# Kernel optimization log

Hardware: AMD Instinct MI355X
Metric: run time of the kernel (lower is better)

Reference implementation:

```python
import jax, jax.numpy as jnp
import numpy as np

B, S, D = 64, 1452, 1024
G, K, R = 288, 4, 32
VIS = 1152  # number of vision patch tokens; tail is S - VIS = 300 text tokens
MAX_TOKENS = 300


def setup_inputs() -> dict:
    key = jax.random.key(0)
    k1, k2, k3, k4 = jax.random.split(key, 4)
    hidden_states = jax.random.normal(k1, (B, S, D), dtype=jnp.float32)
    attention_mask = jnp.ones((B, S), dtype=jnp.int32)
    # all batches share the same vision patch range [0, VIS-1]
    patch_range_list = jnp.tile(jnp.array([[0, VIS - 1]], dtype=jnp.int32), (B, 1))
    base = jnp.broadcast_to(jnp.arange(VIS, dtype=jnp.int32).reshape(1, G, K), (B, G, K))
    drop = jax.random.uniform(k2, (B, G, K)) < 0.1
    patch_indices_list_list = jnp.where(drop, jnp.int32(-1), base)
    rem = jax.random.randint(k3, (B, R), 0, VIS, dtype=jnp.int32)
    rem = jnp.where(jax.random.uniform(k4, (B, R)) < 0.25, jnp.int32(-1), rem)
    return {
        "hidden_states": hidden_states,
        "attention_mask": attention_mask,
        "patch_range_list": patch_range_list,
        "patch_indices_list_list": patch_indices_list_list,
        "remove_index_list_list": rem,
    }


def reference(hidden_states, attention_mask, patch_range_list, patch_indices_list_list, remove_index_list_list):
    Bn, Sn, Dn = hidden_states.shape
    _, Gn, Kn = patch_indices_list_list.shape
    # vision_end_token_index is taken from batch 0 in the original and used for a
    # shape-defining slice; treat as static (identical across batches here).
    vis_end = int(patch_range_list[0, 1]) + 1

    start = patch_range_list[:, 0]            # [B]
    end = patch_range_list[:, 1]              # [B]
    L = end - start + 1                       # [B] length of sliced hidden_state

    idx = patch_indices_list_list             # [B,G,K]
    mask = idx != -1                          # [B,G,K]
    # remove_index_list: drop -1 padding (map to -2 sentinel so it never matches)
    rem = jnp.where(remove_index_list_list == -1, jnp.int32(-2), remove_index_list_list)  # [B,R]
    in_rem = (idx[..., None] == rem[:, None, None, :]).any(-1)  # torch.isin, [B,G,K]
    mask = mask & ~in_rem

    # torch gather with -1 wraps to the last element of the SLICED hidden_state;
    # replicate exactly (note: the original sums wrapped/removed entries too).
    idx_w = jnp.where(idx >= 0, idx, idx + L[:, None, None])
    gidx = start[:, None, None] + idx_w       # absolute indices into hidden_states
    gathered = jnp.take_along_axis(
        hidden_states, gidx.reshape(Bn, Gn * Kn, 1), axis=1
    ).reshape(Bn, Gn, Kn, Dn)

    cnt = mask.sum(-1)                        # [B,G] divisor = count of kept entries
    pooled = gathered.sum(2) / jnp.maximum(cnt, 1)[..., None].astype(hidden_states.dtype)

    # rows with no valid entries are dropped; survivors are written right-aligned
    valid = mask.any(-1)                      # [B,G]
    n_valid = valid.sum(1)                    # [B]
    rank = jnp.cumsum(valid, axis=1) - 1      # 0-based rank among valid rows
    pos = jnp.where(valid, MAX_TOKENS - n_valid[:, None] + rank, MAX_TOKENS)  # OOB -> drop
    bidx = jnp.arange(Bn)[:, None]

    out_head = jnp.zeros((Bn, MAX_TOKENS, Dn), hidden_states.dtype).at[bidx, pos].set(pooled, mode="drop")
    att_head = jnp.zeros((Bn, MAX_TOKENS), attention_mask.dtype).at[bidx, pos].set(1, mode="drop")

    outputs = jnp.concatenate([out_head, hidden_states[:, vis_end:]], axis=1)
    outputs_attention = jnp.concatenate([att_head, attention_mask[:, vis_end:]], axis=1)
    return outputs, outputs_attention
```

## Files before the change

kernel.cpp:

```cpp
#include <hip/hip_runtime.h>
#include <hip/hip_bf16.h>

#define Bn 64
#define Sn 1452
#define Dn 1024
#define Gn 288
#define Kn 4
#define Rn 32
#define MAXT 300

typedef float f32x4 __attribute__((ext_vector_type(4)));

__global__ void __launch_bounds__(512)
phaseA_kernel(const int* __restrict__ idx,
              const int* __restrict__ rem,
              const int* __restrict__ attn,
              int* __restrict__ cnt_ws,
              int* __restrict__ gor_ws,
              int* __restrict__ nv_ws,
              float* __restrict__ att_out,
              int vis_end, int T) {
    const int b = blockIdx.x;
    const int tid = threadIdx.x;

    __shared__ int s_rem[Rn];
    __shared__ int s_wsum[8];

    if (tid < Rn) {
        int r = rem[b * Rn + tid];
        s_rem[tid] = (r == -1) ? -2 : r;
    }
    __syncthreads();

    int cnt = 0;
    if (tid < Gn) {
#pragma unroll
        for (int k = 0; k < Kn; ++k) {
            int v = idx[(b * Gn + tid) * Kn + k];
            bool m = (v != -1);
            if (m) {
#pragma unroll
                for (int r = 0; r < Rn; ++r) {
                    if (v == s_rem[r]) { m = false; }
                }
            }
            cnt += m ? 1 : 0;
        }
        cnt_ws[b * Gn + tid] = cnt;
    }

    const int valid = (tid < Gn && cnt > 0) ? 1 : 0;
    const unsigned long long m = __ballot(valid);
    const int lane = tid & 63;
    const int w = tid >> 6;
    if (lane == 0) s_wsum[w] = __popcll(m);
    __syncthreads();

    int off = 0, tot = 0;
#pragma unroll
    for (int i = 0; i < 8; ++i) {
        int v = s_wsum[i];
        tot += v;
        if (i < w) off += v;
    }
    if (valid) {
        int rank = off + __popcll(m & ((1ull << lane) - 1ull));
        gor_ws[b * Gn + rank] = tid;
    }
    if (tid == 0) nv_ws[b] = tot;

    const int nvalid = tot;
    for (int t = tid; t < T; t += 512) {
        float v;
        if (t < MAXT) {
            v = (t >= MAXT - nvalid) ? 1.0f : 0.0f;
        } else {
            v = (float)attn[b * Sn + vis_end + (t - MAXT)];
        }
        att_out[(size_t)b * T + t] = v;
    }
}

__global__ void __launch_bounds__(256)
rows_kernel(const float* __restrict__ hs,
            const int* __restrict__ idx,
            const int* __restrict__ pr,
            const int* __restrict__ cnt_ws,
            const int* __restrict__ gor_ws,
            const int* __restrict__ nv_ws,
            float* __restrict__ out,
            int vis_end, int T, int nheadblk, int tail4) {
    const int x = blockIdx.x;
    const int b = blockIdx.y;
    const int tid = threadIdx.x;

    if (x >= nheadblk) {
        const int c = x - nheadblk;
        const f32x4* src = (const f32x4*)(hs + ((size_t)b * Sn + vis_end) * Dn);
        f32x4* dst = (f32x4*)(out + ((size_t)b * T + MAXT) * Dn);

        const int base = c * 1024;
        f32x4 v0, v1, v2, v3;
        int e0 = base + 0 * 256 + tid;
        int e1 = base + 1 * 256 + tid;
        int e2 = base + 2 * 256 + tid;
        int e3 = base + 3 * 256 + tid;
        bool p0 = e0 < tail4, p1 = e1 < tail4, p2 = e2 < tail4, p3 = e3 < tail4;
        if (p0) v0 = __builtin_nontemporal_load(&src[e0]);
        if (p1) v1 = __builtin_nontemporal_load(&src[e1]);
        if (p2) v2 = __builtin_nontemporal_load(&src[e2]);
        if (p3) v3 = __builtin_nontemporal_load(&src[e3]);
        if (p0) __builtin_nontemporal_store(v0, &dst[e0]);
        if (p1) __builtin_nontemporal_store(v1, &dst[e1]);
        if (p2) __builtin_nontemporal_store(v2, &dst[e2]);
        if (p3) __builtin_nontemporal_store(v3, &dst[e3]);
        return;
    }

    const int nvalid = nv_ws[b];
    const int zcut = MAXT - nvalid;
    const int start = pr[b * 2];
    const int L = pr[b * 2 + 1] - start + 1;

#pragma unroll
    for (int i = 0; i < 2; ++i) {
        const int t = 2 * x + i;
        if (t >= MAXT) break;
        f32x4* outp = (f32x4*)(out + ((size_t)b * T + t) * Dn);
        if (t < zcut) {
            f32x4 z = {0.f, 0.f, 0.f, 0.f};
            __builtin_nontemporal_store(z, &outp[tid]);
            continue;
        }
        const int g = gor_ws[b * Gn + (t - zcut)];
        f32x4 acc = {0.f, 0.f, 0.f, 0.f};
#pragma unroll
        for (int k = 0; k < Kn; ++k) {
            int v = idx[(b * Gn + g) * Kn + k];
            int w = (v >= 0) ? v : v + L;
            const f32x4* row = (const f32x4*)(hs + ((size_t)b * Sn + start + w) * Dn);
            acc += row[tid];
        }
        const int c = cnt_ws[b * Gn + g];
        const float scale = 1.0f / (float)((c > 1) ? c : 1);
        acc *= scale;
        __builtin_nontemporal_store(acc, &outp[tid]);
    }
}

extern "C" void kernel_launch(void* const* d_in, const int* in_sizes, int n_in,
                              void* d_out, int out_size, void* d_ws, size_t ws_size,
                              hipStream_t stream) {
    const float* hs  = (const float*)d_in[0];
    const int* attn  = (const int*)d_in[1];
    const int* pr    = (const int*)d_in[2];
    const int* idx   = (const int*)d_in[3];
    const int* rem   = (const int*)d_in[4];

    float* out = (float*)d_out;

    const int T = out_size / (Bn * (Dn + 1));
    const int vis_end = Sn - (T - MAXT);

    float* att_out = out + (size_t)Bn * T * Dn;

    int* cnt_ws = (int*)d_ws;
    int* gor_ws = cnt_ws + Bn * Gn;
    int* nv_ws  = gor_ws + Bn * Gn;

    const int tail_rows = T - MAXT;
    const int tail4 = tail_rows * (Dn / 4);
    const int ntail = (tail_rows + 3) / 4;
    const int nheadblk = (MAXT + 1) / 2;

    phaseA_kernel<<<Bn, 512, 0, stream>>>(idx, rem, attn, cnt_ws, gor_ws, nv_ws,
                                          att_out, vis_end, T);
    rows_kernel<<<dim3(nheadblk + ntail, Bn), 256, 0, stream>>>(
        hs, idx, pr, cnt_ws, gor_ws, nv_ws, out, vis_end, T, nheadblk, tail4);
}
```

Baseline: 83.05 us.

## Fuse mask/rank computation into row kernel, recomputing per block in shared memory

Removes the separate phase-A kernel and its global workspace by having every head block recompute the per-batch keep counts, validity ballots and compacted group order in shared memory, then gather and pool its two rows. Tail-copy blocks now also write the attention-mask tail. This eliminates one launch and the inter-kernel dependency, but each of the 150 head blocks per batch redundantly runs the 288x4x32 remove-index comparison and adds two barriers before its memory work.

```diff
diff --git a/kernel.cpp b/kernel.cpp
--- a/kernel.cpp
+++ b/kernel.cpp
@@ -11,94 +11,28 @@
 
 typedef float f32x4 __attribute__((ext_vector_type(4)));
 
-__global__ void __launch_bounds__(512)
-phaseA_kernel(const int* __restrict__ idx,
+__global__ void __launch_bounds__(256)
+fused2_kernel(const float* __restrict__ hs,
+              const int* __restrict__ idx,
+              const int* __restrict__ pr,
               const int* __restrict__ rem,
               const int* __restrict__ attn,
-              int* __restrict__ cnt_ws,
-              int* __restrict__ gor_ws,
-              int* __restrict__ nv_ws,
+              float* __restrict__ out,
               float* __restrict__ att_out,
-              int vis_end, int T) {
-    const int b = blockIdx.x;
-    const int tid = threadIdx.x;
-
-    __shared__ int s_rem[Rn];
-    __shared__ int s_wsum[8];
-
-    if (tid < Rn) {
-        int r = rem[b * Rn + tid];
-        s_rem[tid] = (r == -1) ? -2 : r;
-    }
-    __syncthreads();
-
-    int cnt = 0;
-    if (tid < Gn) {
-#pragma unroll
-        for (int k = 0; k < Kn; ++k) {
-            int v = idx[(b * Gn + tid) * Kn + k];
-            bool m = (v != -1);
-            if (m) {
-#pragma unroll
-                for (int r = 0; r < Rn; ++r) {
-                    if (v == s_rem[r]) { m = false; }
-                }
-            }
-            cnt += m ? 1 : 0;
-        }
-        cnt_ws[b * Gn + tid] = cnt;
-    }
-
-    const int valid = (tid < Gn && cnt > 0) ? 1 : 0;
-    const unsigned long long m = __ballot(valid);
-    const int lane = tid & 63;
-    const int w = tid >> 6;
-    if (lane == 0) s_wsum[w] = __popcll(m);
-    __syncthreads();
-
-    int off = 0, tot = 0;
-#pragma unroll
-    for (int i = 0; i < 8; ++i) {
-        int v = s_wsum[i];
-        tot += v;
-        if (i < w) off += v;
-    }
-    if (valid) {
-        int rank = off + __popcll(m & ((1ull << lane) - 1ull));
-        gor_ws[b * Gn + rank] = tid;
-    }
-    if (tid == 0) nv_ws[b] = tot;
-
-    const int nvalid = tot;
-    for (int t = tid; t < T; t += 512) {
-        float v;
-        if (t < MAXT) {
-            v = (t >= MAXT - nvalid) ? 1.0f : 0.0f;
-        } else {
-            v = (float)attn[b * Sn + vis_end + (t - MAXT)];
-        }
-        att_out[(size_t)b * T + t] = v;
-    }
-}
-
-__global__ void __launch_bounds__(256)
-rows_kernel(const float* __restrict__ hs,
-            const int* __restrict__ idx,
-            const int* __restrict__ pr,
-            const int* __restrict__ cnt_ws,
-            const int* __restrict__ gor_ws,
-            const int* __restrict__ nv_ws,
-            float* __restrict__ out,
-            int vis_end, int T, int nheadblk, int tail4) {
+              int vis_end, int T, int nheadblk, int tail4, int tailrows) {
     const int x = blockIdx.x;
     const int b = blockIdx.y;
     const int tid = threadIdx.x;
 
     if (x >= nheadblk) {
         const int c = x - nheadblk;
+        if (tid < 4) {
+            int tr = c * 4 + tid;
+            if (tr < tailrows)
+                att_out[(size_t)b * T + MAXT + tr] = (float)attn[b * Sn + vis_end + tr];
+        }
         const f32x4* src = (const f32x4*)(hs + ((size_t)b * Sn + vis_end) * Dn);
         f32x4* dst = (f32x4*)(out + ((size_t)b * T + MAXT) * Dn);
-
         const int base = c * 1024;
         f32x4 v0, v1, v2, v3;
         int e0 = base + 0 * 256 + tid;
@@ -117,34 +51,102 @@
         return;
     }
 
-    const int nvalid = nv_ws[b];
+    __shared__ int s_rem[Rn];
+    __shared__ unsigned long long s_mask[5];
+    __shared__ int s_wsum[5];
+    __shared__ short s_gor[Gn];
+    __shared__ char s_cnt[Gn];
+
+    const int lane = tid & 63;
+    const int w = tid >> 6;
+
+    if (tid < Rn) {
+        int r = rem[b * Rn + tid];
+        s_rem[tid] = (r == -1) ? -2 : r;
+    }
+    __syncthreads();
+
+    int cnt1 = 0;
+    {
+        const int g = tid;
+#pragma unroll
+        for (int k = 0; k < Kn; ++k) {
+            int v = idx[(b * Gn + g) * Kn + k];
+            bool m = (v != -1);
+#pragma unroll
+            for (int r = 0; r < Rn; ++r) m = m && (v != s_rem[r]);
+            cnt1 += m ? 1 : 0;
+        }
+        s_cnt[g] = (char)cnt1;
+    }
+    int cnt2 = 0;
+    if (tid < Gn - 256) {
+        const int g = 256 + tid;
+#pragma unroll
+        for (int k = 0; k < Kn; ++k) {
+            int v = idx[(b * Gn + g) * Kn + k];
+            bool m = (v != -1);
+#pragma unroll
+            for (int r = 0; r < Rn; ++r) m = m && (v != s_rem[r]);
+            cnt2 += m ? 1 : 0;
+        }
+        s_cnt[g] = (char)cnt2;
+    }
+
+    unsigned long long m1 = __ballot(cnt1 > 0);
+    if (lane == 0) { s_mask[w] = m1; s_wsum[w] = __popcll(m1); }
+    if (w == 0) {
+        unsigned long long m2 = __ballot(tid < Gn - 256 && cnt2 > 0);
+        if (lane == 0) { s_mask[4] = m2; s_wsum[4] = __popcll(m2); }
+    }
+    __syncthreads();
+
+    int pre[5], acc = 0;
+#pragma unroll
+    for (int i = 0; i < 5; ++i) { pre[i] = acc; acc += s_wsum[i]; }
+    const int nvalid = acc;
     const int zcut = MAXT - nvalid;
+
+    if (cnt1 > 0) {
+        int rank = pre[w] + __popcll(s_mask[w] & ((1ull << lane) - 1ull));
+        s_gor[rank] = (short)tid;
+    }
+    if (tid < Gn - 256 && cnt2 > 0) {
+        int rank = pre[4] + __popcll(s_mask[4] & ((1ull << lane) - 1ull));
+        s_gor[rank] = (short)(256 + tid);
+    }
+    __syncthreads();
+
+    if (tid < 2) {
+        int t = 2 * x + tid;
+        att_out[(size_t)b * T + t] = (t >= zcut) ? 1.0f : 0.0f;
+    }
+
     const int start = pr[b * 2];
     const int L = pr[b * 2 + 1] - start + 1;
 
 #pragma unroll
     for (int i = 0; i < 2; ++i) {
         const int t = 2 * x + i;
-        if (t >= MAXT) break;
         f32x4* outp = (f32x4*)(out + ((size_t)b * T + t) * Dn);
         if (t < zcut) {
             f32x4 z = {0.f, 0.f, 0.f, 0.f};
             __builtin_nontemporal_store(z, &outp[tid]);
             continue;
         }
-        const int g = gor_ws[b * Gn + (t - zcut)];
-        f32x4 acc = {0.f, 0.f, 0.f, 0.f};
+        const int g = s_gor[t - zcut];
+        f32x4 a = {0.f, 0.f, 0.f, 0.f};
 #pragma unroll
         for (int k = 0; k < Kn; ++k) {
             int v = idx[(b * Gn + g) * Kn + k];
-            int w = (v >= 0) ? v : v + L;
-            const f32x4* row = (const f32x4*)(hs + ((size_t)b * Sn + start + w) * Dn);
-            acc += row[tid];
+            int wi = (v >= 0) ? v : v + L;
+            const f32x4* row = (const f32x4*)(hs + ((size_t)b * Sn + start + wi) * Dn);
+            a += row[tid];
         }
-        const int c = cnt_ws[b * Gn + g];
+        const int c = (int)s_cnt[g];
         const float scale = 1.0f / (float)((c > 1) ? c : 1);
-        acc *= scale;
-        __builtin_nontemporal_store(acc, &outp[tid]);
+        a *= scale;
+        __builtin_nontemporal_store(a, &outp[tid]);
     }
 }
 
@@ -164,17 +166,11 @@
 
     float* att_out = out + (size_t)Bn * T * Dn;
 
-    int* cnt_ws = (int*)d_ws;
-    int* gor_ws = cnt_ws + Bn * Gn;
-    int* nv_ws  = gor_ws + Bn * Gn;
-
-    const int tail_rows = T - MAXT;
-    const int tail4 = tail_rows * (Dn / 4);
-    const int ntail = (tail_rows + 3) / 4;
+    const int tailrows = T - MAXT;
+    const int tail4 = tailrows * (Dn / 4);
+    const int ntail = (tailrows + 3) / 4;
     const int nheadblk = (MAXT + 1) / 2;
 
-    phaseA_kernel<<<Bn, 512, 0, stream>>>(idx, rem, attn, cnt_ws, gor_ws, nv_ws,
-                                          att_out, vis_end, T);
-    rows_kernel<<<dim3(nheadblk + ntail, Bn), 256, 0, stream>>>(
-        hs, idx, pr, cnt_ws, gor_ws, nv_ws, out, vis_end, T, nheadblk, tail4);
+    fused2_kernel<<<dim3(nheadblk + ntail, Bn), 256, 0, stream>>>(
+        hs, idx, pr, rem, attn, out, att_out, vis_end, T, nheadblk, tail4, tailrows);
 }
```

Result: faster. 79.54 us (-4.2%).
